# Optimization experiments

Hardware: AMD Instinct MI355X
Metric: run time of the kernel (lower is better)

Reference implementation:

```python
import jax, jax.numpy as jnp
import numpy as np

DIAGNUM, MEDNUM, PRONUM, FEATDIM = 50000, 20000, 40000, 128
N1 = DIAGNUM + MEDNUM  # 70000
N2 = PRONUM + MEDNUM   # 60000
NNZ1, NNZ2 = 1_120_000, 960_000


def setup_inputs() -> dict:
    key = jax.random.key(0)
    ks = jax.random.split(key, 10)
    return {
        "adj1_rows": jax.random.randint(ks[0], (2, NNZ1), 0, N1, dtype=jnp.int32),
        "adj1_cols": jax.random.randint(ks[1], (2, NNZ1), 0, N1, dtype=jnp.int32),
        "adj1_vals": jax.random.uniform(ks[2], (2, NNZ1), dtype=jnp.float32),
        "adj2_rows": jax.random.randint(ks[3], (2, NNZ2), 0, N2, dtype=jnp.int32),
        "adj2_cols": jax.random.randint(ks[4], (2, NNZ2), 0, N2, dtype=jnp.int32),
        "adj2_vals": jax.random.uniform(ks[5], (2, NNZ2), dtype=jnp.float32),
        "dEmbed": jax.random.normal(ks[6], (DIAGNUM, FEATDIM), dtype=jnp.float32),
        "mEmbed": jax.random.normal(ks[7], (MEDNUM, FEATDIM), dtype=jnp.float32),
        "pEmbed": jax.random.normal(ks[8], (PRONUM, FEATDIM), dtype=jnp.float32),
        "inter": jax.random.uniform(ks[9], (1,), dtype=jnp.float32),
    }


def _spmm(rows, cols, vals, x, n):
    # sparse COO matmul: out[r] += vals * x[cols]
    msgs = vals[:, None] * x[cols]  # [nnz, d]
    return jax.ops.segment_sum(msgs, rows, num_segments=n)


def _gcn_layer(rows, cols, vals, x, n):
    h = _spmm(rows, cols, vals, x, n)
    h = jnp.where(h >= 0, h, 0.5 * h)  # LeakyReLU(0.5)
    return jax.nn.relu(h)              # extra F.relu in the loop


def reference(adj1_rows, adj1_cols, adj1_vals,
              adj2_rows, adj2_cols, adj2_vals,
              dEmbed, mEmbed, pEmbed, inter):
    diagnum, pronum = dEmbed.shape[0], pEmbed.shape[0]
    e1 = jnp.concatenate([dEmbed, mEmbed], axis=0)  # [N1, d]
    e2 = jnp.concatenate([pEmbed, mEmbed], axis=0)  # [N2, d]
    n1, n2 = e1.shape[0], e2.shape[0]
    # Original loops never extend lats1/lats2, so every iteration uses the
    # initial embeddings; each adj[i] contribution appears twice (j=0,1).
    g1 = jnp.zeros_like(e1)
    g2 = jnp.zeros_like(e2)
    for _j in range(2):
        for i in range(2):
            g1 = g1 + _gcn_layer(adj1_rows[i], adj1_cols[i], adj1_vals[i], e1, n1)
            g2 = g2 + _gcn_layer(adj2_rows[i], adj2_cols[i], adj2_vals[i], e2, n2)
    mEmbed_gcn_1 = g1[diagnum:]
    dEmbed_gcn = g1[:diagnum]
    mEmbed_gcn_2 = g2[pronum:]
    pEmbed_gcn = g2[:pronum]
    mEmbed_out = inter * mEmbed_gcn_1 + (1.0 - inter) * mEmbed_gcn_2
    return (mEmbed_out, dEmbed_gcn, pEmbed_gcn)
```

## Files before the change

### kernel.cpp

```cpp
#include <hip/hip_runtime.h>
#include <hip/hip_fp16.h>

#define DIAGNUM 50000
#define MEDNUM  20000
#define PRONUM  40000
#define FEATDIM 128
#define N1 (DIAGNUM + MEDNUM)
#define N2 (PRONUM + MEDNUM)
#define NNZ1 1120000
#define NNZ2 960000
#define NTOT (2 * N1 + 2 * N2)
#define NNZTOT (2 * NNZ1 + 2 * NNZ2)
#define NBUCK ((NTOT + 255) >> 8)
#define L1_THREADS 512
#define L1_CHUNK 8192
#define L1_ITERS (L1_CHUNK / L1_THREADS)
#define L1_BLOCKS ((NNZTOT + L1_CHUNK - 1) / L1_CHUNK)

typedef unsigned short ushort_t;

__device__ __forceinline__ int edge_idx(int i, const int* __restrict__ a1r,
                                        const int* __restrict__ a2r) {
    if (i < 2 * NNZ1) {
        return ((i < NNZ1) ? 0 : N1) + a1r[i];
    } else {
        int j = i - 2 * NNZ1;
        return 2 * N1 + ((j < NNZ2) ? 0 : N2) + a2r[j];
    }
}

__global__ __launch_bounds__(256) void count_buckets_kernel(
        const int* __restrict__ a1r, const int* __restrict__ a2r,
        int* __restrict__ bucketCnt) {
    __shared__ int lh[NBUCK];
    for (int b = threadIdx.x; b < NBUCK; b += 256) lh[b] = 0;
    __syncthreads();
    int stride = gridDim.x * 256;
    for (int i = blockIdx.x * 256 + threadIdx.x; i < NNZTOT; i += stride)
        atomicAdd(&lh[edge_idx(i, a1r, a2r) >> 8], 1);
    __syncthreads();
    for (int b = threadIdx.x; b < NBUCK; b += 256) {
        int h = lh[b];
        if (h) atomicAdd(&bucketCnt[b], h);
    }
}

__global__ __launch_bounds__(256) void scan_buckets_kernel(
        const int* __restrict__ bucketCnt, int* __restrict__ bucketOff,
        int* __restrict__ cursor) {
    __shared__ int s[256];
    int t = threadIdx.x;
    int vals[4];
    int sum = 0;
#pragma unroll
    for (int k = 0; k < 4; k++) {
        int b = t * 4 + k;
        vals[k] = (b < NBUCK) ? bucketCnt[b] : 0;
        sum += vals[k];
    }
    s[t] = sum;
    __syncthreads();
    for (int off = 1; off < 256; off <<= 1) {
        int y = (t >= off) ? s[t - off] : 0;
        __syncthreads();
        s[t] += y;
        __syncthreads();
    }
    int run = s[t] - sum;
#pragma unroll
    for (int k = 0; k < 4; k++) {
        int b = t * 4 + k;
        if (b < NBUCK) {
            bucketOff[b] = run;
            cursor[b] = run;
            run += vals[k];
        }
    }
    if (t == 255) bucketOff[NBUCK] = run;
}

__global__ __launch_bounds__(L1_THREADS) void lvl1_scatter_kernel(
        const int* __restrict__ a1r, const int* __restrict__ a1c,
        const float* __restrict__ a1v,
        const int* __restrict__ a2r, const int* __restrict__ a2c,
        const float* __restrict__ a2v,
        int* __restrict__ cursor, int2* __restrict__ lvl1) {
    __shared__ int lh[NBUCK];
    for (int b = threadIdx.x; b < NBUCK; b += L1_THREADS) lh[b] = 0;
    __syncthreads();
    int base = blockIdx.x * L1_CHUNK;
    int end  = min(base + L1_CHUNK, NNZTOT);
    int idxv[L1_ITERS];
    {
        int it = 0;
        for (int i = base + threadIdx.x; i < end; i += L1_THREADS, it++) {
            int idx = edge_idx(i, a1r, a2r);
            idxv[it] = idx;
            atomicAdd(&lh[idx >> 8], 1);
        }
    }
    __syncthreads();
    for (int b = threadIdx.x; b < NBUCK; b += L1_THREADS) {
        int h = lh[b];
        lh[b] = h ? atomicAdd(&cursor[b], h) : 0;
    }
    __syncthreads();
    {
        int it = 0;
        for (int i = base + threadIdx.x; i < end; i += L1_THREADS, it++) {
            int col;
            float val;
            if (i < 2 * NNZ1) {
                col = a1c[i];
                val = a1v[i];
            } else {
                int j = i - 2 * NNZ1;
                col = a2c[j];
                val = a2v[j];
            }
            int idx = idxv[it];
            int pos = atomicAdd(&lh[idx >> 8], 1);
            lvl1[pos] = make_int2(((idx & 255) << 17) | col, __float_as_int(val));
        }
    }
}

__global__ __launch_bounds__(256) void lvl2_sort_kernel(
        const int2* __restrict__ lvl1, const int* __restrict__ bucketOff,
        int* __restrict__ binned, int* __restrict__ rpe) {
    __shared__ int cnt[256];
    __shared__ int sc[256];
    int b = blockIdx.x;
    int t = threadIdx.x;
    int s0 = bucketOff[b];
    int e0 = bucketOff[b + 1];
    cnt[t] = 0;
    __syncthreads();
    for (int k = s0 + t; k < e0; k += 256)
        atomicAdd(&cnt[lvl1[k].x >> 17], 1);
    __syncthreads();
    int v = cnt[t];
    sc[t] = v;
    __syncthreads();
    for (int off = 1; off < 256; off <<= 1) {
        int y = (t >= off) ? sc[t - off] : 0;
        __syncthreads();
        sc[t] += y;
        __syncthreads();
    }
    int incl = sc[t];
    int excl = incl - v;
    int idx = (b << 8) + t;
    if (idx < NTOT) rpe[idx + 1] = s0 + incl;
    cnt[t] = excl;
    __syncthreads();
    for (int k = s0 + t; k < e0; k += 256) {
        int2 rec = lvl1[k];
        int rl  = rec.x >> 17;
        int col = rec.x & 0x1FFFF;
        unsigned hv = __half_as_ushort(__float2half(__int_as_float(rec.y)));
        int pos = atomicAdd(&cnt[rl], 1);
        binned[s0 + pos] = (int)((hv << 17) | (unsigned)col);
    }
}

#define TOT8 ((DIAGNUM + MEDNUM + PRONUM) * (FEATDIM / 8))

__device__ __forceinline__ ushort_t f2h(float x) {
    return __half_as_ushort(__float2half(x));
}

__global__ __launch_bounds__(256) void convert_emb_kernel(
        const float* __restrict__ dE, const float* __restrict__ mE,
        const float* __restrict__ pE,
        ushort_t* __restrict__ emb1, ushort_t* __restrict__ emb2) {
    int t8 = blockIdx.x * 256 + threadIdx.x;
    if (t8 >= TOT8) return;
    long flat = (long)t8 * 8;
    const float* src;
    ushort_t* dst;
    ushort_t* dst2 = nullptr;
    if (flat < (long)DIAGNUM * FEATDIM) {
        src = dE + flat;
        dst = emb1 + flat;
    } else if (flat < (long)(DIAGNUM + MEDNUM) * FEATDIM) {
        long o = flat - (long)DIAGNUM * FEATDIM;
        src = mE + o;
        dst  = emb1 + (long)DIAGNUM * FEATDIM + o;
        dst2 = emb2 + (long)PRONUM * FEATDIM + o;
    } else {
        long o = flat - (long)(DIAGNUM + MEDNUM) * FEATDIM;
        src = pE + o;
        dst = emb2 + o;
    }
    float4 a = *reinterpret_cast<const float4*>(src);
    float4 b = *reinterpret_cast<const float4*>(src + 4);
    int4 w;
    w.x = (int)((unsigned)f2h(a.x) | ((unsigned)f2h(a.y) << 16));
    w.y = (int)((unsigned)f2h(a.z) | ((unsigned)f2h(a.w) << 16));
    w.z = (int)((unsigned)f2h(b.x) | ((unsigned)f2h(b.y) << 16));
    w.w = (int)((unsigned)f2h(b.z) | ((unsigned)f2h(b.w) << 16));
    *reinterpret_cast<int4*>(dst) = w;
    if (dst2) *reinterpret_cast<int4*>(dst2) = w;
}


__device__ __forceinline__ void fma8(float acc[8], float v, int4 h) {
    union U { int4 i; __half2 h2[4]; } u;
    u.i = h;
#pragma unroll
    for (int j = 0; j < 4; j++) {
        float2 f = __half22float2(u.h2[j]);
        acc[2 * j]     = fmaf(v, f.x, acc[2 * j]);
        acc[2 * j + 1] = fmaf(v, f.y, acc[2 * j + 1]);
    }
}

__device__ __forceinline__ float rec_val(unsigned rec) {
    return __half2float(__ushort_as_half((unsigned short)(rec >> 17)));
}

__device__ __forceinline__ void gather8(int s, int e,
                                        const int* __restrict__ binned,
                                        int q, int sub16,
                                        const ushort_t* __restrict__ emb,
                                        float acc[8]) {
    int k = s + q;
    for (; k + 4 < e; k += 8) {
        unsigned r0 = (unsigned)binned[k];
        unsigned r1 = (unsigned)binned[k + 4];
        const int4* b0 = reinterpret_cast<const int4*>(emb + ((size_t)(r0 & 0x1FFFFu) << 7));
        const int4* b1 = reinterpret_cast<const int4*>(emb + ((size_t)(r1 & 0x1FFFFu) << 7));
        int4 h0 = b0[sub16];
        int4 h1 = b1[sub16];
        fma8(acc, rec_val(r0), h0);
        fma8(acc, rec_val(r1), h1);
    }
    for (; k < e; k += 4) {
        unsigned r0 = (unsigned)binned[k];
        const int4* b0 = reinterpret_cast<const int4*>(emb + ((size_t)(r0 & 0x1FFFFu) << 7));
        int4 h0 = b0[sub16];
        fma8(acc, rec_val(r0), h0);
    }
}

__global__ __launch_bounds__(256) void fused_gcn_kernel(
        const int* __restrict__ rpe,
        const int* __restrict__ binned,
        const ushort_t* __restrict__ emb,
        const float* __restrict__ inter,
        float* __restrict__ out_d, float* __restrict__ out_p,
        float* __restrict__ out_m, int graph) {
    int gtid = blockIdx.x * blockDim.x + threadIdx.x;
    int w     = gtid >> 6;
    int lane  = gtid & 63;
    int q     = lane >> 4;
    int sub16 = lane & 15;

    const int *rpA, *rpB;
    int nrows;
    if (graph) { nrows = N1; rpA = rpe + w; rpB = rpe + N1 + w; }
    else       { nrows = N2; rpA = rpe + 2 * N1 + w; rpB = rpe + 2 * N1 + N2 + w; }
    if (w >= nrows) return;

    float aA[8] = {0, 0, 0, 0, 0, 0, 0, 0};
    float aB[8] = {0, 0, 0, 0, 0, 0, 0, 0};
    gather8(rpA[0], rpA[1], binned, q, sub16, emb, aA);
    gather8(rpB[0], rpB[1], binned, q, sub16, emb, aB);

#pragma unroll
    for (int j = 0; j < 8; j++) {
        aA[j] += __shfl_xor(aA[j], 16);
        aA[j] += __shfl_xor(aA[j], 32);
        aB[j] += __shfl_xor(aB[j], 16);
        aB[j] += __shfl_xor(aB[j], 32);
    }

    if (lane >= 16) return;

    float r[8];
#pragma unroll
    for (int j = 0; j < 8; j++)
        r[j] = 2.f * (fmaxf(aA[j], 0.f) + fmaxf(aB[j], 0.f));

    float4 lo = make_float4(r[0], r[1], r[2], r[3]);
    float4 hi = make_float4(r[4], r[5], r[6], r[7]);

    if (graph) {
        if (w < DIAGNUM) {
            float4* dst = reinterpret_cast<float4*>(out_d + (size_t)w * FEATDIM);
            dst[sub16 * 2]     = lo;
            dst[sub16 * 2 + 1] = hi;
        } else {
            float t = *inter;
            float4* dst = reinterpret_cast<float4*>(
                out_m + (size_t)(w - DIAGNUM) * FEATDIM);
            float4 o0 = dst[sub16 * 2];
            float4 o1 = dst[sub16 * 2 + 1];
            o0.x = fmaf(t, lo.x, o0.x); o0.y = fmaf(t, lo.y, o0.y);
            o0.z = fmaf(t, lo.z, o0.z); o0.w = fmaf(t, lo.w, o0.w);
            o1.x = fmaf(t, hi.x, o1.x); o1.y = fmaf(t, hi.y, o1.y);
            o1.z = fmaf(t, hi.z, o1.z); o1.w = fmaf(t, hi.w, o1.w);
            dst[sub16 * 2]     = o0;
            dst[sub16 * 2 + 1] = o1;
        }
    } else {
        if (w < PRONUM) {
            float4* dst = reinterpret_cast<float4*>(out_p + (size_t)w * FEATDIM);
            dst[sub16 * 2]     = lo;
            dst[sub16 * 2 + 1] = hi;
        } else {
            float sc = 1.0f - *inter;
            lo.x *= sc; lo.y *= sc; lo.z *= sc; lo.w *= sc;
            hi.x *= sc; hi.y *= sc; hi.z *= sc; hi.w *= sc;
            float4* dst = reinterpret_cast<float4*>(
                out_m + (size_t)(w - PRONUM) * FEATDIM);
            dst[sub16 * 2]     = lo;
            dst[sub16 * 2 + 1] = hi;
        }
    }
}


extern "C" void kernel_launch(void* const* d_in, const int* in_sizes, int n_in,
                              void* d_out, int out_size, void* d_ws, size_t ws_size,
                              hipStream_t stream) {
    const int*   a1r = (const int*)d_in[0];
    const int*   a1c = (const int*)d_in[1];
    const float* a1v = (const float*)d_in[2];
    const int*   a2r = (const int*)d_in[3];
    const int*   a2c = (const int*)d_in[4];
    const float* a2v = (const float*)d_in[5];
    const float* dE  = (const float*)d_in[6];
    const float* mE  = (const float*)d_in[7];
    const float* pE  = (const float*)d_in[8];
    const float* inter = (const float*)d_in[9];

    float* out   = (float*)d_out;
    float* out_m = out;
    float* out_d = out + (size_t)MEDNUM * FEATDIM;
    float* out_p = out_d + (size_t)DIAGNUM * FEATDIM;

    char* ws = (char*)d_ws;
    int* binned = (int*)ws;          ws += (size_t)NNZTOT * 4;
    char* regionB = ws;              ws += (size_t)NNZTOT * 8;
    int2*     lvl1 = (int2*)regionB;
    ushort_t* emb1 = (ushort_t*)regionB;
    ushort_t* emb2 = emb1 + (size_t)N1 * FEATDIM;
    int* rpe       = (int*)ws;       ws += (((size_t)(NTOT + 1) * 4 + 15) & ~15ull);
    int* bucketCnt = (int*)ws;       ws += (size_t)NBUCK * 4;
    int* bucketOff = (int*)ws;       ws += (size_t)(NBUCK + 1) * 4;
    int* cursor    = (int*)ws;       ws += (size_t)NBUCK * 4;

    const int BLK = 256;

    hipMemsetAsync(bucketCnt, 0, (size_t)NBUCK * sizeof(int), stream);
    hipMemsetAsync(rpe, 0, sizeof(int), stream);

    count_buckets_kernel<<<512, BLK, 0, stream>>>(a1r, a2r, bucketCnt);
    scan_buckets_kernel<<<1, BLK, 0, stream>>>(bucketCnt, bucketOff, cursor);
    lvl1_scatter_kernel<<<L1_BLOCKS, L1_THREADS, 0, stream>>>(
        a1r, a1c, a1v, a2r, a2c, a2v, cursor, lvl1);
    lvl2_sort_kernel<<<NBUCK, BLK, 0, stream>>>(lvl1, bucketOff, binned, rpe);

    convert_emb_kernel<<<(TOT8 + BLK - 1) / BLK, BLK, 0, stream>>>(
        dE, mE, pE, emb1, emb2);

    fused_gcn_kernel<<<(N2 + 3) / 4, BLK, 0, stream>>>(
        rpe, binned, emb2, inter, out_d, out_p, out_m, 0);
    fused_gcn_kernel<<<(N1 + 3) / 4, BLK, 0, stream>>>(
        rpe, binned, emb1, inter, out_d, out_p, out_m, 1);
}
```

Before: 255.0 us.

## Merge both GCN graph launches, split level-1 buffer, use nontemporal loads/stores

Both graphs now go through a single fused_gcn launch. The shared medication rows are combined through float atomicAdd into a zero-initialised out_m, which replaces the second launch's read-modify-write. The level-1 sort buffer is split into an int column array and a half-precision value array, so the float-to-half conversion moves earlier and fewer bytes move. Nontemporal loads and stores are applied to streaming index/value reads and output writes. The costs are an extra memset and per-element float atomics on the medication rows, which also make the summation order nondeterministic.

```diff
diff --git a/kernel.cpp b/kernel.cpp
--- a/kernel.cpp
+++ b/kernel.cpp
@@ -18,14 +18,15 @@
 #define L1_BLOCKS ((NNZTOT + L1_CHUNK - 1) / L1_CHUNK)
 
 typedef unsigned short ushort_t;
+typedef float f32x4 __attribute__((ext_vector_type(4)));
 
 __device__ __forceinline__ int edge_idx(int i, const int* __restrict__ a1r,
                                         const int* __restrict__ a2r) {
     if (i < 2 * NNZ1) {
-        return ((i < NNZ1) ? 0 : N1) + a1r[i];
+        return ((i < NNZ1) ? 0 : N1) + __builtin_nontemporal_load(a1r + i);
     } else {
         int j = i - 2 * NNZ1;
-        return 2 * N1 + ((j < NNZ2) ? 0 : N2) + a2r[j];
+        return 2 * N1 + ((j < NNZ2) ? 0 : N2) + __builtin_nontemporal_load(a2r + j);
     }
 }
 
@@ -84,7 +85,8 @@
         const float* __restrict__ a1v,
         const int* __restrict__ a2r, const int* __restrict__ a2c,
         const float* __restrict__ a2v,
-        int* __restrict__ cursor, int2* __restrict__ lvl1) {
+        int* __restrict__ cursor,
+        int* __restrict__ l1cols, ushort_t* __restrict__ l1vals) {
     __shared__ int lh[NBUCK];
     for (int b = threadIdx.x; b < NBUCK; b += L1_THREADS) lh[b] = 0;
     __syncthreads();
@@ -111,22 +113,24 @@
             int col;
             float val;
             if (i < 2 * NNZ1) {
-                col = a1c[i];
-                val = a1v[i];
+                col = __builtin_nontemporal_load(a1c + i);
+                val = __builtin_nontemporal_load(a1v + i);
             } else {
                 int j = i - 2 * NNZ1;
-                col = a2c[j];
-                val = a2v[j];
+                col = __builtin_nontemporal_load(a2c + j);
+                val = __builtin_nontemporal_load(a2v + j);
             }
             int idx = idxv[it];
             int pos = atomicAdd(&lh[idx >> 8], 1);
-            lvl1[pos] = make_int2(((idx & 255) << 17) | col, __float_as_int(val));
+            l1cols[pos] = ((idx & 255) << 17) | col;
+            l1vals[pos] = __half_as_ushort(__float2half(val));
         }
     }
 }
 
 __global__ __launch_bounds__(256) void lvl2_sort_kernel(
-        const int2* __restrict__ lvl1, const int* __restrict__ bucketOff,
+        const int* __restrict__ l1cols, const ushort_t* __restrict__ l1vals,
+        const int* __restrict__ bucketOff,
         int* __restrict__ binned, int* __restrict__ rpe) {
     __shared__ int cnt[256];
     __shared__ int sc[256];
@@ -137,7 +141,7 @@
     cnt[t] = 0;
     __syncthreads();
     for (int k = s0 + t; k < e0; k += 256)
-        atomicAdd(&cnt[lvl1[k].x >> 17], 1);
+        atomicAdd(&cnt[__builtin_nontemporal_load(l1cols + k) >> 17], 1);
     __syncthreads();
     int v = cnt[t];
     sc[t] = v;
@@ -155,10 +159,10 @@
     cnt[t] = excl;
     __syncthreads();
     for (int k = s0 + t; k < e0; k += 256) {
-        int2 rec = lvl1[k];
-        int rl  = rec.x >> 17;
-        int col = rec.x & 0x1FFFF;
-        unsigned hv = __half_as_ushort(__float2half(__int_as_float(rec.y)));
+        int c  = __builtin_nontemporal_load(l1cols + k);
+        unsigned hv = __builtin_nontemporal_load(l1vals + k);
+        int rl  = c >> 17;
+        int col = c & 0x1FFFF;
         int pos = atomicAdd(&cnt[rl], 1);
         binned[s0 + pos] = (int)((hv << 17) | (unsigned)col);
     }
@@ -227,8 +231,8 @@
                                         float acc[8]) {
     int k = s + q;
     for (; k + 4 < e; k += 8) {
-        unsigned r0 = (unsigned)binned[k];
-        unsigned r1 = (unsigned)binned[k + 4];
+        unsigned r0 = (unsigned)__builtin_nontemporal_load(binned + k);
+        unsigned r1 = (unsigned)__builtin_nontemporal_load(binned + k + 4);
         const int4* b0 = reinterpret_cast<const int4*>(emb + ((size_t)(r0 & 0x1FFFFu) << 7));
         const int4* b1 = reinterpret_cast<const int4*>(emb + ((size_t)(r1 & 0x1FFFFu) << 7));
         int4 h0 = b0[sub16];
@@ -237,31 +241,45 @@
         fma8(acc, rec_val(r1), h1);
     }
     for (; k < e; k += 4) {
-        unsigned r0 = (unsigned)binned[k];
+        unsigned r0 = (unsigned)__builtin_nontemporal_load(binned + k);
         const int4* b0 = reinterpret_cast<const int4*>(emb + ((size_t)(r0 & 0x1FFFFu) << 7));
         int4 h0 = b0[sub16];
         fma8(acc, rec_val(r0), h0);
     }
 }
 
+__device__ __forceinline__ void nt_store4(float* p, float a, float b,
+                                          float c, float d) {
+    f32x4 v = {a, b, c, d};
+    __builtin_nontemporal_store(v, reinterpret_cast<f32x4*>(p));
+}
+
 __global__ __launch_bounds__(256) void fused_gcn_kernel(
         const int* __restrict__ rpe,
         const int* __restrict__ binned,
-        const ushort_t* __restrict__ emb,
+        const ushort_t* __restrict__ emb1, const ushort_t* __restrict__ emb2,
         const float* __restrict__ inter,
         float* __restrict__ out_d, float* __restrict__ out_p,
-        float* __restrict__ out_m, int graph) {
+        float* __restrict__ out_m) {
     int gtid = blockIdx.x * blockDim.x + threadIdx.x;
     int w     = gtid >> 6;
     int lane  = gtid & 63;
     int q     = lane >> 4;
     int sub16 = lane & 15;
-
+    if (w >= N1 + N2) return;
+
+    const ushort_t* emb;
     const int *rpA, *rpB;
-    int nrows;
-    if (graph) { nrows = N1; rpA = rpe + w; rpB = rpe + N1 + w; }
-    else       { nrows = N2; rpA = rpe + 2 * N1 + w; rpB = rpe + 2 * N1 + N2 + w; }
-    if (w >= nrows) return;
+    int r, graph;
+    if (w < N2) {
+        graph = 0; r = w; emb = emb2;
+        rpA = rpe + 2 * N1 + r;
+        rpB = rpe + 2 * N1 + N2 + r;
+    } else {
+        graph = 1; r = w - N2; emb = emb1;
+        rpA = rpe + r;
+        rpB = rpe + N1 + r;
+    }
 
     float aA[8] = {0, 0, 0, 0, 0, 0, 0, 0};
     float aB[8] = {0, 0, 0, 0, 0, 0, 0, 0};
@@ -278,45 +296,32 @@
 
     if (lane >= 16) return;
 
-    float r[8];
+    float res[8];
 #pragma unroll
     for (int j = 0; j < 8; j++)
-        r[j] = 2.f * (fmaxf(aA[j], 0.f) + fmaxf(aB[j], 0.f));
-
-    float4 lo = make_float4(r[0], r[1], r[2], r[3]);
-    float4 hi = make_float4(r[4], r[5], r[6], r[7]);
+        res[j] = 2.f * (fmaxf(aA[j], 0.f) + fmaxf(aB[j], 0.f));
 
     if (graph) {
-        if (w < DIAGNUM) {
-            float4* dst = reinterpret_cast<float4*>(out_d + (size_t)w * FEATDIM);
-            dst[sub16 * 2]     = lo;
-            dst[sub16 * 2 + 1] = hi;
+        if (r < DIAGNUM) {
+            float* dst = out_d + (size_t)r * FEATDIM + sub16 * 8;
+            nt_store4(dst,     res[0], res[1], res[2], res[3]);
+            nt_store4(dst + 4, res[4], res[5], res[6], res[7]);
         } else {
             float t = *inter;
-            float4* dst = reinterpret_cast<float4*>(
-                out_m + (size_t)(w - DIAGNUM) * FEATDIM);
-            float4 o0 = dst[sub16 * 2];
-            float4 o1 = dst[sub16 * 2 + 1];
-            o0.x = fmaf(t, lo.x, o0.x); o0.y = fmaf(t, lo.y, o0.y);
-            o0.z = fmaf(t, lo.z, o0.z); o0.w = fmaf(t, lo.w, o0.w);
-            o1.x = fmaf(t, hi.x, o1.x); o1.y = fmaf(t, hi.y, o1.y);
-            o1.z = fmaf(t, hi.z, o1.z); o1.w = fmaf(t, hi.w, o1.w);
-            dst[sub16 * 2]     = o0;
-            dst[sub16 * 2 + 1] = o1;
+            float* dst = out_m + (size_t)(r - DIAGNUM) * FEATDIM + sub16 * 8;
+#pragma unroll
+            for (int j = 0; j < 8; j++) atomicAdd(dst + j, t * res[j]);
         }
     } else {
-        if (w < PRONUM) {
-            float4* dst = reinterpret_cast<float4*>(out_p + (size_t)w * FEATDIM);
-            dst[sub16 * 2]     = lo;
-            dst[sub16 * 2 + 1] = hi;
+        if (r < PRONUM) {
+            float* dst = out_p + (size_t)r * FEATDIM + sub16 * 8;
+            nt_store4(dst,     res[0], res[1], res[2], res[3]);
+            nt_store4(dst + 4, res[4], res[5], res[6], res[7]);
         } else {
             float sc = 1.0f - *inter;
-            lo.x *= sc; lo.y *= sc; lo.z *= sc; lo.w *= sc;
-            hi.x *= sc; hi.y *= sc; hi.z *= sc; hi.w *= sc;
-            float4* dst = reinterpret_cast<float4*>(
-                out_m + (size_t)(w - PRONUM) * FEATDIM);
-            dst[sub16 * 2]     = lo;
-            dst[sub16 * 2 + 1] = hi;
+            float* dst = out_m + (size_t)(r - PRONUM) * FEATDIM + sub16 * 8;
+#pragma unroll
+            for (int j = 0; j < 8; j++) atomicAdd(dst + j, sc * res[j]);
         }
     }
 }
@@ -344,7 +349,8 @@
     char* ws = (char*)d_ws;
     int* binned = (int*)ws;          ws += (size_t)NNZTOT * 4;
     char* regionB = ws;              ws += (size_t)NNZTOT * 8;
-    int2*     lvl1 = (int2*)regionB;
+    int*      l1cols = (int*)regionB;
+    ushort_t* l1vals = (ushort_t*)(regionB + (size_t)NNZTOT * 4);
     ushort_t* emb1 = (ushort_t*)regionB;
     ushort_t* emb2 = emb1 + (size_t)N1 * FEATDIM;
     int* rpe       = (int*)ws;       ws += (((size_t)(NTOT + 1) * 4 + 15) & ~15ull);
@@ -354,20 +360,21 @@
 
     const int BLK = 256;
 
-    hipMemsetAsync(bucketCnt, 0, (size_t)NBUCK * sizeof(int), stream);
-    hipMemsetAsync(rpe, 0, sizeof(int), stream);
+    (void)hipMemsetAsync(bucketCnt, 0, (size_t)NBUCK * sizeof(int), stream);
+    (void)hipMemsetAsync(rpe, 0, sizeof(int), stream);
+    (void)hipMemsetAsync(out_m, 0, (size_t)MEDNUM * FEATDIM * sizeof(float), stream);
 
     count_buckets_kernel<<<512, BLK, 0, stream>>>(a1r, a2r, bucketCnt);
     scan_buckets_kernel<<<1, BLK, 0, stream>>>(bucketCnt, bucketOff, cursor);
     lvl1_scatter_kernel<<<L1_BLOCKS, L1_THREADS, 0, stream>>>(
-        a1r, a1c, a1v, a2r, a2c, a2v, cursor, lvl1);
-    lvl2_sort_kernel<<<NBUCK, BLK, 0, stream>>>(lvl1, bucketOff, binned, rpe);
+        a1r, a1c, a1v, a2r, a2c, a2v, cursor, l1cols, l1vals);
+    lvl2_sort_kernel<<<NBUCK, BLK, 0, stream>>>(l1cols, l1vals, bucketOff,
+                                                binned, rpe);
 
     convert_emb_kernel<<<(TOT8 + BLK - 1) / BLK, BLK, 0, stream>>>(
         dE, mE, pE, emb1, emb2);
 
-    fused_gcn_kernel<<<(N2 + 3) / 4, BLK, 0, stream>>>(
-        rpe, binned, emb2, inter, out_d, out_p, out_m, 0);
-    fused_gcn_kernel<<<(N1 + 3) / 4, BLK, 0, stream>>>(
-        rpe, binned, emb1, inter, out_d, out_p, out_m, 1);
-}
+    int nrows = N1 + N2;
+    fused_gcn_kernel<<<(nrows + 3) / 4, BLK, 0, stream>>>(
+        rpe, binned, emb1, emb2, inter, out_d, out_p, out_m);
+}
```

Result: slower. 445.8 us (+74.8%).
